# Kernel tuning notes

Hardware: AMD Instinct MI355X
Metric: run time of the kernel (lower is better)

The kernel has to match this reference:

```python
import math
import jax, jax.numpy as jnp
import numpy as np

NUM_EXPERTS = 8
TOP_K = 2
HIDDEN = 1024
INTERMEDIATE = 4096
CAPACITY_FACTOR = 1.0


def setup_inputs() -> dict:
    key = jax.random.key(0)
    k1, k2, k3, k4, k5, k6 = jax.random.split(key, 6)
    T = 8192
    hidden_states = jax.random.normal(k1, (T, HIDDEN), dtype=jnp.float32)
    # router affinities (already softmax-normalized in the real pipeline; uniform here is fine for correctness)
    expert_affinities = jax.random.uniform(k2, (T, NUM_EXPERTS), dtype=jnp.float32)
    expert_index = jax.random.randint(k3, (T, TOP_K), 0, NUM_EXPERTS, dtype=jnp.int32)
    scale = 0.02
    gate_w = jax.random.normal(k4, (NUM_EXPERTS, HIDDEN, INTERMEDIATE), dtype=jnp.float32) * scale
    up_w = jax.random.normal(k5, (NUM_EXPERTS, HIDDEN, INTERMEDIATE), dtype=jnp.float32) * scale
    down_w = jax.random.normal(k6, (NUM_EXPERTS, INTERMEDIATE, HIDDEN), dtype=jnp.float32) * scale
    return {"hidden_states": hidden_states, "expert_affinities": expert_affinities,
            "gate_w": gate_w, "up_w": up_w, "down_w": down_w, "expert_index": expert_index}


def reference(hidden_states, expert_affinities, gate_w, up_w, down_w, expert_index):
    T, H = hidden_states.shape
    E, K = NUM_EXPERTS, TOP_K
    C = min(math.ceil(T * K * CAPACITY_FACTOR / E), T)  # expert capacity (static)

    # top_k-hot expert mask (T, E)
    expert_mask = jax.nn.one_hot(expert_index, E, dtype=jnp.float32).sum(axis=1)
    # 1-indexed position of each token within each expert's queue
    position_in_expert = jnp.cumsum(expert_mask, axis=0)
    # capacity-based token dropping
    expert_mask = jnp.where(position_in_expert > C, 0.0, expert_mask)

    # masked (and L1-normalized) affinities of chosen experts
    aff_masked = jnp.where(expert_mask == 0, 0.0, expert_affinities)
    denom = jnp.maximum(jnp.sum(jnp.abs(aff_masked), axis=1, keepdims=True), 1e-12)
    aff_masked = aff_masked / denom  # normalize_top_k_affinities=True

    # flattened slot index per (token, expert): expert e occupies slots [e*C, (e+1)*C)
    offsets = jnp.arange(E, dtype=jnp.float32) * C
    pos_off = position_in_expert + offsets[None, :]
    pos_off = jnp.where(expert_mask == 0, 0.0, pos_off)

    # (T, K) slot index (1-based; 0 == dropped)
    perm_idx = jnp.take_along_axis(pos_off, expert_index, axis=1).astype(jnp.int32)

    # invert permutation: slot -> token (1-based; slot 0 collects all dropped tokens, then discarded)
    tok_ids = jnp.broadcast_to((jnp.arange(T, dtype=jnp.int32) + 1)[:, None], (T, K)).reshape(-1)
    assign = jnp.zeros(E * C + 1, dtype=jnp.int32).at[perm_idx.reshape(-1)].set(tok_ids)
    assign = assign[1:].reshape(E, C) - 1
    assign = jnp.maximum(assign, 0)          # empty slots read token 0 (output unused)
    perm_idx = jnp.maximum(perm_idx - 1, 0)  # dropped tokens read slot 0 (affinity == 0)

    # gather tokens into per-expert blocks and run grouped GLU MLP
    x_e = hidden_states[assign]  # (E, C, H)
    gate = jax.nn.silu(jnp.einsum('ech,ehi->eci', x_e, gate_w))
    inter = gate * jnp.einsum('ech,ehi->eci', x_e, up_w)  # (E, C, I)
    out_e = jnp.einsum('eci,eih->ech', inter, down_w)      # (E, C, H)
    permuted_output = out_e.reshape(E * C, H)

    # combine: gather each token's top_k expert outputs weighted by masked affinities
    out_k = permuted_output[perm_idx]                                   # (T, K, H)
    aff_k = jnp.take_along_axis(aff_masked, expert_index, axis=1)       # (T, K)
    return jnp.sum(out_k * aff_k[:, :, None], axis=1)
```

## Files before the change

kernel.cpp:

```cpp
#include <hip/hip_runtime.h>
#include <stdint.h>

#define T_TOK 8192
#define HID   1024
#define INTER 4096
#define NE    8
#define TOPK  2
#define CAP   2048
#define EC    (NE * CAP)


typedef __attribute__((ext_vector_type(8))) short bf16x8;
typedef __attribute__((ext_vector_type(4))) float f32x4;

static __device__ __forceinline__ unsigned short f2bf(float f) {
    union { float f; unsigned u; } a; a.f = f;
    unsigned r = a.u + 0x7FFFu + ((a.u >> 16) & 1u);
    return (unsigned short)(r >> 16);
}
static __device__ __forceinline__ float bf2f(unsigned short b) {
    union { unsigned u; float f; } a; a.u = ((unsigned)b) << 16;
    return a.f;
}

static __device__ __forceinline__ void gload(const unsigned short* g, unsigned short* l) {
    __builtin_amdgcn_global_load_lds((__attribute__((address_space(1))) void*)(uintptr_t)g,
                                     (__attribute__((address_space(3))) void*)l, 16, 0, 0);
}

#define BAR() do { asm volatile("" ::: "memory"); __builtin_amdgcn_s_barrier(); asm volatile("" ::: "memory"); } while (0)
#define WAITVM(N) asm volatile("s_waitcnt vmcnt(" #N ")" ::: "memory")

__global__ __launch_bounds__(512) void route_kernel(const int* __restrict__ eidx,
                                                    int* __restrict__ perm,
                                                    int* __restrict__ assign) {
    int tid = threadIdx.x;
    for (int i = tid; i < EC; i += 512) assign[i] = 0;
    __syncthreads();
    int e = tid >> 6;
    int lane = tid & 63;
    const int TPL = T_TOK / 64;
    int t0 = lane * TPL;
    int cnt = 0;
    for (int t = t0; t < t0 + TPL; ++t) {
        int e0 = eidx[t * 2], e1 = eidx[t * 2 + 1];
        cnt += (e0 == e) + (e1 == e);
    }
    int incl = cnt;
    #pragma unroll
    for (int off = 1; off < 64; off <<= 1) {
        int n = __shfl_up(incl, off, 64);
        if (lane >= off) incl += n;
    }
    int run = incl - cnt;
    for (int t = t0; t < t0 + TPL; ++t) {
        int e0 = eidx[t * 2], e1 = eidx[t * 2 + 1];
        int c = (e0 == e) + (e1 == e);
        if (c) {
            run += c;
            int pos = run;
            bool keep = (pos <= CAP);
            int pi = keep ? (pos + e * CAP) : 0;
            if (e0 == e) perm[t * 2]     = pi;
            if (e1 == e) perm[t * 2 + 1] = pi;
            if (keep) assign[pi - 1] = t;
        }
    }
}

__global__ __launch_bounds__(256) void transpose_cvt2(const float* __restrict__ in0,
                                                      unsigned short* __restrict__ out0,
                                                      const float* __restrict__ in1,
                                                      unsigned short* __restrict__ out1) {
    __shared__ unsigned short tile[64][68];
    int z = blockIdx.z;
    const float* in = (z < 8) ? in0 : in1;
    unsigned short* out = (z < 8) ? out0 : out1;
    int e = z & 7;
    const int R = HID, Cc = INTER;
    const float* inp = in + (size_t)e * R * Cc;
    unsigned short* outp = out + (size_t)e * R * Cc;
    int c0 = blockIdx.x * 64, r0 = blockIdx.y * 64;
    int t = threadIdx.x;
    int x = t & 15;
    int ry = t >> 4;
    #pragma unroll
    for (int j = 0; j < 4; ++j) {
        int row = ry + 16 * j;
        float4 v = *(const float4*)(inp + (size_t)(r0 + row) * Cc + c0 + 4 * x);
        ushort4 o;
        o.x = f2bf(v.x); o.y = f2bf(v.y); o.z = f2bf(v.z); o.w = f2bf(v.w);
        *(ushort4*)&tile[row][4 * x] = o;
    }
    __syncthreads();
    #pragma unroll
    for (int j = 0; j < 4; ++j) {
        int oc = ry + 16 * j;
        ushort4 o;
        o.x = tile[4 * x + 0][oc];
        o.y = tile[4 * x + 1][oc];
        o.z = tile[4 * x + 2][oc];
        o.w = tile[4 * x + 3][oc];
        *(ushort4*)(outp + (size_t)(c0 + oc) * R + r0 + 4 * x) = o;
    }
}

__global__ __launch_bounds__(256) void transpose_cvt(const float* __restrict__ in,
                                                     unsigned short* __restrict__ out,
                                                     int R, int Cc) {
    __shared__ unsigned short tile[64][68];
    int e = blockIdx.z;
    const float* inp = in + (size_t)e * R * Cc;
    unsigned short* outp = out + (size_t)e * R * Cc;
    int c0 = blockIdx.x * 64, r0 = blockIdx.y * 64;
    int t = threadIdx.x;
    int x = t & 15;
    int ry = t >> 4;
    #pragma unroll
    for (int j = 0; j < 4; ++j) {
        int row = ry + 16 * j;
        float4 v = *(const float4*)(inp + (size_t)(r0 + row) * Cc + c0 + 4 * x);
        ushort4 o;
        o.x = f2bf(v.x); o.y = f2bf(v.y); o.z = f2bf(v.z); o.w = f2bf(v.w);
        *(ushort4*)&tile[row][4 * x] = o;
    }
    __syncthreads();
    #pragma unroll
    for (int j = 0; j < 4; ++j) {
        int oc = ry + 16 * j;
        ushort4 o;
        o.x = tile[4 * x + 0][oc];
        o.y = tile[4 * x + 1][oc];
        o.z = tile[4 * x + 2][oc];
        o.w = tile[4 * x + 3][oc];
        *(ushort4*)(outp + (size_t)(c0 + oc) * R + r0 + 4 * x) = o;
    }
}

__global__ __launch_bounds__(256) void gather_cvt(const float* __restrict__ hs,
                                                  const int* __restrict__ assign,
                                                  unsigned short* __restrict__ xe) {
    int s = blockIdx.x;
    int tok = assign[s];
    const float* src = hs + (size_t)tok * HID;
    unsigned short* dst = xe + (size_t)s * HID;
    int h = threadIdx.x * 4;
    float4 v = *(const float4*)(src + h);
    ushort4 o;
    o.x = f2bf(v.x); o.y = f2bf(v.y); o.z = f2bf(v.z); o.w = f2bf(v.w);
    *(ushort4*)(dst + h) = o;
}


#define BUFE 12288

#define MFMA16(ACC, O, B0, B1) \
    _Pragma("unroll") \
    for (int mi = 0; mi < 8; ++mi) { \
        ACC[mi][O]     = __builtin_amdgcn_mfma_f32_16x16x32_bf16(aF[mi], B0, ACC[mi][O], 0, 0, 0); \
        ACC[mi][O + 1] = __builtin_amdgcn_mfma_f32_16x16x32_bf16(aF[mi], B1, ACC[mi][O + 1], 0, 0, 0); \
    }

#define LOAD_AF(rd) \
    _Pragma("unroll") \
    for (int mi = 0; mi < 8; ++mi) aF[mi] = *(const bf16x8*)((rd) + aRd + mi * 512);

__global__ __launch_bounds__(256, 2) void gateup_gemm(const unsigned short* __restrict__ Xe,
                                                      const unsigned short* __restrict__ WgT,
                                                      const unsigned short* __restrict__ WuT,
                                                      unsigned short* __restrict__ interB) {
    extern __shared__ __align__(16) unsigned short smemU[];
    const int K = HID;
    const int NT = K / 32;

    int e  = blockIdx.x;
    int m0 = blockIdx.y * 256;
    int n0 = blockIdx.z * 64;

    int tid = threadIdx.x;
    int lane = tid & 63, w = tid >> 6;
    int lm = lane & 15, hi = lane >> 4;
    int wm = w >> 1, wn = w & 1;

    const int swz  = (hi ^ ((lm >> 1) & 3)) << 3;
    const int aRd  = (wm * 128 + lm) * 32 + swz;
    const int r1Rd = 8192  + (wn * 32 + lm) * 32 + swz;
    const int r2Rd = 10240 + (wn * 32 + lm) * 32 + swz;

    int sr = lane >> 2;
    int sc = ((lane & 3) ^ ((lane >> 3) & 3)) << 3;
    const unsigned short* aS = Xe  + ((size_t)e * CAP   + m0 + w * 64 + sr) * K + sc;
    const unsigned short* gS = WgT + ((size_t)e * INTER + n0 + w * 16 + sr) * K + sc;
    const unsigned short* uS = WuT + ((size_t)e * INTER + n0 + w * 16 + sr) * K + sc;
    const int dA = w * 2048;
    const int dG = 8192  + w * 512;
    const int dU = 10240 + w * 512;

    f32x4 zero = {0.f, 0.f, 0.f, 0.f};
    f32x4 accG[8][2], accU[8][2];
    #pragma unroll
    for (int i = 0; i < 8; ++i) {
        accG[i][0] = zero; accG[i][1] = zero;
        accU[i][0] = zero; accU[i][1] = zero;
    }

    unsigned short* p0 = smemU;
    unsigned short* p1 = smemU + BUFE;
    unsigned short* p2 = smemU + 2 * BUFE;

    {
        #pragma unroll
        for (int j = 0; j < 4; ++j) gload(aS + (size_t)j * 16 * K, p0 + dA + j * 512);
        gload(gS, p0 + dG); gload(uS, p0 + dU);
        #pragma unroll
        for (int j = 0; j < 4; ++j) gload(aS + (size_t)j * 16 * K + 32, p1 + dA + j * 512);
        gload(gS + 32, p1 + dG); gload(uS + 32, p1 + dU);
        WAITVM(7);
        BAR();
    }

    bf16x8 aF[8];
    int gk = 64;
    for (int t = 0; t < NT - 2; ++t) {
        const unsigned short* rd = p0;
        unsigned short* wr = p2;
        LOAD_AF(rd);
        bf16x8 b0 = *(const bf16x8*)(rd + r1Rd);
        bf16x8 b1 = *(const bf16x8*)(rd + r1Rd + 512);
        #pragma unroll
        for (int j = 0; j < 4; ++j) gload(aS + (size_t)j * 16 * K + gk, wr + dA + j * 512);
        gload(gS + gk, wr + dG);
        WAITVM(11);
        BAR();
        __builtin_amdgcn_s_setprio(1);
        MFMA16(accG, 0, b0, b1);
        __builtin_amdgcn_s_setprio(0);
        BAR();
        b0 = *(const bf16x8*)(rd + r2Rd);
        b1 = *(const bf16x8*)(rd + r2Rd + 512);
        gload(uS + gk, wr + dU);
        WAITVM(7);
        BAR();
        __builtin_amdgcn_s_setprio(1);
        MFMA16(accU, 0, b0, b1);
        __builtin_amdgcn_s_setprio(0);
        BAR();
        unsigned short* tmp = p0; p0 = p1; p1 = p2; p2 = tmp;
        gk += 32;
    }
    {
        const unsigned short* rd = p0;
        LOAD_AF(rd);
        bf16x8 b0 = *(const bf16x8*)(rd + r1Rd);
        bf16x8 b1 = *(const bf16x8*)(rd + r1Rd + 512);
        WAITVM(6);
        BAR();
        MFMA16(accG, 0, b0, b1);
        BAR();
        b0 = *(const bf16x8*)(rd + r2Rd);
        b1 = *(const bf16x8*)(rd + r2Rd + 512);
        WAITVM(1);
        BAR();
        MFMA16(accU, 0, b0, b1);
        BAR();
    }
    {
        const unsigned short* rd = p1;
        LOAD_AF(rd);
        bf16x8 b0 = *(const bf16x8*)(rd + r1Rd);
        bf16x8 b1 = *(const bf16x8*)(rd + r1Rd + 512);
        WAITVM(0);
        BAR();
        MFMA16(accG, 0, b0, b1);
        BAR();
        b0 = *(const bf16x8*)(rd + r2Rd);
        b1 = *(const bf16x8*)(rd + r2Rd + 512);
        MFMA16(accU, 0, b0, b1);
    }

    __syncthreads();
    unsigned short* bounce = smemU;
    #pragma unroll
    for (int mi = 0; mi < 8; ++mi)
        #pragma unroll
        for (int nf = 0; nf < 2; ++nf) {
            f32x4 g4 = accG[mi][nf], u4 = accU[mi][nf];
            #pragma unroll
            for (int r = 0; r < 4; ++r) {
                int row = wm * 128 + mi * 16 + hi * 4 + r;
                int col = wn * 32 + nf * 16 + lm;
                float g = g4[r];
                float s = g / (1.f + __expf(-g)) * u4[r];
                bounce[row * 72 + col] = f2bf(s);
            }
        }
    __syncthreads();
    {
        unsigned short* Op = interB + ((size_t)e * CAP + m0) * INTER + n0;
        int rr = tid >> 3, cc = (tid & 7) * 8;
        #pragma unroll
        for (int j = 0; j < 8; ++j) {
            int row = rr + 32 * j;
            bf16x8 v = *(const bf16x8*)&bounce[row * 72 + cc];
            *(bf16x8*)(Op + (size_t)row * INTER + cc) = v;
        }
    }
}

__global__ __launch_bounds__(256, 2) void down_gemm(const unsigned short* __restrict__ interB,
                                                    const unsigned short* __restrict__ WdT,
                                                    unsigned short* __restrict__ pout) {
    extern __shared__ __align__(16) unsigned short smemU[];
    const int K = INTER;
    const int NT = K / 32;

    int e  = blockIdx.x;
    int m0 = blockIdx.y * 256;
    int n0 = blockIdx.z * 128;

    int tid = threadIdx.x;
    int lane = tid & 63, w = tid >> 6;
    int lm = lane & 15, hi = lane >> 4;
    int wm = w >> 1, wn = w & 1;

    const int swz  = (hi ^ ((lm >> 1) & 3)) << 3;
    const int aRd  = (wm * 128 + lm) * 32 + swz;
    const int r1Rd = 8192  + (wn * 32 + lm) * 32 + swz;
    const int r2Rd = 10240 + (wn * 32 + lm) * 32 + swz;

    int sr = lane >> 2;
    int sc = ((lane & 3) ^ ((lane >> 3) & 3)) << 3;
    const unsigned short* aS = interB + ((size_t)e * CAP + m0 + w * 64 + sr) * K + sc;
    int rb1 = (w >> 1) * 64 + (w & 1) * 16;
    const unsigned short* b1S = WdT + ((size_t)e * HID + n0 + rb1 + sr) * K + sc;
    const unsigned short* b2S = WdT + ((size_t)e * HID + n0 + rb1 + 32 + sr) * K + sc;
    const int dA = w * 2048;
    const int d1 = 8192  + w * 512;
    const int d2 = 10240 + w * 512;

    f32x4 zero = {0.f, 0.f, 0.f, 0.f};
    f32x4 acc[8][4];
    #pragma unroll
    for (int i = 0; i < 8; ++i)
        #pragma unroll
        for (int j = 0; j < 4; ++j) acc[i][j] = zero;

    unsigned short* p0 = smemU;
    unsigned short* p1 = smemU + BUFE;
    unsigned short* p2 = smemU + 2 * BUFE;

    {
        #pragma unroll
        for (int j = 0; j < 4; ++j) gload(aS + (size_t)j * 16 * K, p0 + dA + j * 512);
        gload(b1S, p0 + d1); gload(b2S, p0 + d2);
        #pragma unroll
        for (int j = 0; j < 4; ++j) gload(aS + (size_t)j * 16 * K + 32, p1 + dA + j * 512);
        gload(b1S + 32, p1 + d1); gload(b2S + 32, p1 + d2);
        WAITVM(7);
        BAR();
    }

    bf16x8 aF[8];
    int gk = 64;
    for (int t = 0; t < NT - 2; ++t) {
        const unsigned short* rd = p0;
        unsigned short* wr = p2;
        LOAD_AF(rd);
        bf16x8 b0 = *(const bf16x8*)(rd + r1Rd);
        bf16x8 b1 = *(const bf16x8*)(rd + r1Rd + 512);
        #pragma unroll
        for (int j = 0; j < 4; ++j) gload(aS + (size_t)j * 16 * K + gk, wr + dA + j * 512);
        gload(b1S + gk, wr + d1);
        WAITVM(11);
        BAR();
        __builtin_amdgcn_s_setprio(1);
        MFMA16(acc, 0, b0, b1);
        __builtin_amdgcn_s_setprio(0);
        BAR();
        b0 = *(const bf16x8*)(rd + r2Rd);
        b1 = *(const bf16x8*)(rd + r2Rd + 512);
        gload(b2S + gk, wr + d2);
        WAITVM(7);
        BAR();
        __builtin_amdgcn_s_setprio(1);
        MFMA16(acc, 2, b0, b1);
        __builtin_amdgcn_s_setprio(0);
        BAR();
        unsigned short* tmp = p0; p0 = p1; p1 = p2; p2 = tmp;
        gk += 32;
    }
    {
        const unsigned short* rd = p0;
        LOAD_AF(rd);
        bf16x8 b0 = *(const bf16x8*)(rd + r1Rd);
        bf16x8 b1 = *(const bf16x8*)(rd + r1Rd + 512);
        WAITVM(6);
        BAR();
        MFMA16(acc, 0, b0, b1);
        BAR();
        b0 = *(const bf16x8*)(rd + r2Rd);
        b1 = *(const bf16x8*)(rd + r2Rd + 512);
        WAITVM(1);
        BAR();
        MFMA16(acc, 2, b0, b1);
        BAR();
    }
    {
        const unsigned short* rd = p1;
        LOAD_AF(rd);
        bf16x8 b0 = *(const bf16x8*)(rd + r1Rd);
        bf16x8 b1 = *(const bf16x8*)(rd + r1Rd + 512);
        WAITVM(0);
        BAR();
        MFMA16(acc, 0, b0, b1);
        BAR();
        b0 = *(const bf16x8*)(rd + r2Rd);
        b1 = *(const bf16x8*)(rd + r2Rd + 512);
        MFMA16(acc, 2, b0, b1);
    }

    unsigned short* bounce = smemU;
    unsigned short* Op = pout + ((size_t)e * CAP + m0) * HID + n0;
    int rr = tid >> 3, c8 = tid & 7;
    int colp = c8 * 8;
    #pragma unroll
    for (int R = 0; R < 2; ++R) {
        __syncthreads();
        #pragma unroll
        for (int mi = 0; mi < 8; ++mi)
            #pragma unroll
            for (int nf = 0; nf < 2; ++nf) {
                f32x4 a4 = acc[mi][2 * R + nf];
                #pragma unroll
                for (int r = 0; r < 4; ++r) {
                    int row = wm * 128 + mi * 16 + hi * 4 + r;
                    int col = wn * 32 + nf * 16 + lm;
                    bounce[row * 72 + col] = f2bf(a4[r]);
                }
            }
        __syncthreads();
        int gcol = (colp >> 5) * 64 + R * 32 + (colp & 31);
        #pragma unroll
        for (int j = 0; j < 8; ++j) {
            int row = rr + 32 * j;
            bf16x8 v = *(const bf16x8*)&bounce[row * 72 + colp];
            *(bf16x8*)(Op + (size_t)row * HID + gcol) = v;
        }
    }
}

__global__ __launch_bounds__(256) void combine_kernel(const float* __restrict__ aff,
                                                      const int* __restrict__ eidx,
                                                      const int* __restrict__ perm,
                                                      const unsigned short* __restrict__ pout,
                                                      float* __restrict__ out) {
    int t = blockIdx.x;
    int e0 = eidx[t * 2], e1 = eidx[t * 2 + 1];
    int p0 = perm[t * 2], p1 = perm[t * 2 + 1];
    bool k0 = p0 > 0, k1 = p1 > 0;
    float a0 = aff[t * NE + e0], a1 = aff[t * NE + e1];
    float denom = (k0 ? fabsf(a0) : 0.f) + ((e1 != e0 && k1) ? fabsf(a1) : 0.f);
    denom = fmaxf(denom, 1e-12f);
    float w0 = k0 ? a0 / denom : 0.f;
    float w1 = k1 ? a1 / denom : 0.f;
    int s0 = k0 ? p0 - 1 : 0;
    int s1 = k1 ? p1 - 1 : 0;
    int h = threadIdx.x * 4;
    ushort4 v0 = *(const ushort4*)(pout + (size_t)s0 * HID + h);
    ushort4 v1 = *(const ushort4*)(pout + (size_t)s1 * HID + h);
    float4 o;
    o.x = w0 * bf2f(v0.x) + w1 * bf2f(v1.x);
    o.y = w0 * bf2f(v0.y) + w1 * bf2f(v1.y);
    o.z = w0 * bf2f(v0.z) + w1 * bf2f(v1.z);
    o.w = w0 * bf2f(v0.w) + w1 * bf2f(v1.w);
    *(float4*)(out + (size_t)t * HID + h) = o;
}

extern "C" void kernel_launch(void* const* d_in, const int* in_sizes, int n_in,
                              void* d_out, int out_size, void* d_ws, size_t ws_size,
                              hipStream_t stream) {
    (void)in_sizes; (void)n_in; (void)out_size; (void)ws_size;
    const float* hs   = (const float*)d_in[0];
    const float* aff  = (const float*)d_in[1];
    const float* gw   = (const float*)d_in[2];
    const float* uw   = (const float*)d_in[3];
    const float* dw   = (const float*)d_in[4];
    const int*   eidx = (const int*)d_in[5];
    float* out = (float*)d_out;

    char* ws = (char*)d_ws;
    unsigned short* WgT    = (unsigned short*)(ws);
    unsigned short* WuT    = (unsigned short*)(ws + ((size_t)64  << 20));
    unsigned short* WdT    = (unsigned short*)(ws + ((size_t)128 << 20));
    unsigned short* Xe     = (unsigned short*)(ws + ((size_t)192 << 20));
    unsigned short* interB = (unsigned short*)(ws + ((size_t)224 << 20));
    unsigned short* pout   = (unsigned short*)(ws + ((size_t)352 << 20));
    int*            perm   = (int*)           (ws + ((size_t)416 << 20));
    int*            assign = perm + (T_TOK * TOPK);

    static int attr_set = 0;
    if (!attr_set) {
        (void)hipFuncSetAttribute((const void*)gateup_gemm,
                                  hipFuncAttributeMaxDynamicSharedMemorySize, 73728);
        (void)hipFuncSetAttribute((const void*)down_gemm,
                                  hipFuncAttributeMaxDynamicSharedMemorySize, 73728);
        attr_set = 1;
    }

    route_kernel<<<1, 512, 0, stream>>>(eidx, perm, assign);
    transpose_cvt2<<<dim3(INTER / 64, HID / 64, 16), 256, 0, stream>>>(uw, WuT, gw, WgT);
    transpose_cvt<<<dim3(HID / 64, INTER / 64, NE), 256, 0, stream>>>(dw, WdT, INTER, HID);
    gather_cvt<<<EC, 256, 0, stream>>>(hs, assign, Xe);
    gateup_gemm<<<dim3(8, 8, 64), 256, 73728, stream>>>(Xe, WgT, WuT, interB);
    down_gemm<<<dim3(8, 8, 8), 256, 73728, stream>>>(interB, WdT, pout);
    combine_kernel<<<T_TOK, 256, 0, stream>>>(aff, eidx, perm, pout, out);
}
```

Before: 912.0 us.

## Switch expert GEMMs to 32x32x16 MFMA and load B operands directly from global

Both the gate/up and down GEMMs move from 16x16x32 bf16 MFMA tiles to 32x32x16 tiles with 16-wide accumulators. Weight (B) fragments are now read straight from global memory into registers and prefetched one K-step ahead, instead of being staged through LDS. Only the activation tile stays in LDS, which shrinks shared memory per block from 72KB to 48KB and removes one barrier pair per K-step. In exchange, the B reads become uncoalesced per-lane global loads that depend on cache hits, and the epilogue row mapping changes to match the new accumulator layout.

```diff
diff --git a/kernel.cpp b/kernel.cpp
--- a/kernel.cpp
+++ b/kernel.cpp
@@ -12,6 +12,7 @@
 
 typedef __attribute__((ext_vector_type(8))) short bf16x8;
 typedef __attribute__((ext_vector_type(4))) float f32x4;
+typedef __attribute__((ext_vector_type(16))) float f32x16;
 
 static __device__ __forceinline__ unsigned short f2bf(float f) {
     union { float f; unsigned u; } a; a.f = f;
@@ -152,18 +153,7 @@
 }
 
 
-#define BUFE 12288
-
-#define MFMA16(ACC, O, B0, B1) \
-    _Pragma("unroll") \
-    for (int mi = 0; mi < 8; ++mi) { \
-        ACC[mi][O]     = __builtin_amdgcn_mfma_f32_16x16x32_bf16(aF[mi], B0, ACC[mi][O], 0, 0, 0); \
-        ACC[mi][O + 1] = __builtin_amdgcn_mfma_f32_16x16x32_bf16(aF[mi], B1, ACC[mi][O + 1], 0, 0, 0); \
-    }
-
-#define LOAD_AF(rd) \
-    _Pragma("unroll") \
-    for (int mi = 0; mi < 8; ++mi) aF[mi] = *(const bf16x8*)((rd) + aRd + mi * 512);
+#define BUFE 8192
 
 __global__ __launch_bounds__(256, 2) void gateup_gemm(const unsigned short* __restrict__ Xe,
                                                       const unsigned short* __restrict__ WgT,
@@ -179,121 +169,123 @@
 
     int tid = threadIdx.x;
     int lane = tid & 63, w = tid >> 6;
-    int lm = lane & 15, hi = lane >> 4;
+    int r = lane & 31, hi2 = lane >> 5;
     int wm = w >> 1, wn = w & 1;
 
-    const int swz  = (hi ^ ((lm >> 1) & 3)) << 3;
-    const int aRd  = (wm * 128 + lm) * 32 + swz;
-    const int r1Rd = 8192  + (wn * 32 + lm) * 32 + swz;
-    const int r2Rd = 10240 + (wn * 32 + lm) * 32 + swz;
+    int q = (r >> 1) & 3;
+    const int aOff0 = wm * 4096 + r * 32 + ((hi2 ^ q) << 3);
+    const int aOff1 = wm * 4096 + r * 32 + (((2 | hi2) ^ q) << 3);
 
     int sr = lane >> 2;
     int sc = ((lane & 3) ^ ((lane >> 3) & 3)) << 3;
-    const unsigned short* aS = Xe  + ((size_t)e * CAP   + m0 + w * 64 + sr) * K + sc;
-    const unsigned short* gS = WgT + ((size_t)e * INTER + n0 + w * 16 + sr) * K + sc;
-    const unsigned short* uS = WuT + ((size_t)e * INTER + n0 + w * 16 + sr) * K + sc;
+    const unsigned short* aS = Xe + ((size_t)e * CAP + m0 + w * 64 + sr) * K + sc;
     const int dA = w * 2048;
-    const int dG = 8192  + w * 512;
-    const int dU = 10240 + w * 512;
-
-    f32x4 zero = {0.f, 0.f, 0.f, 0.f};
-    f32x4 accG[8][2], accU[8][2];
-    #pragma unroll
-    for (int i = 0; i < 8; ++i) {
-        accG[i][0] = zero; accG[i][1] = zero;
-        accU[i][0] = zero; accU[i][1] = zero;
-    }
+
+    const unsigned short* gP = WgT + ((size_t)e * INTER + n0 + wn * 32 + r) * K + hi2 * 8;
+    const unsigned short* uP = WuT + ((size_t)e * INTER + n0 + wn * 32 + r) * K + hi2 * 8;
+
+    f32x16 accG[4], accU[4];
+    f32x16 zero = {0.f,0.f,0.f,0.f,0.f,0.f,0.f,0.f,0.f,0.f,0.f,0.f,0.f,0.f,0.f,0.f};
+    #pragma unroll
+    for (int i = 0; i < 4; ++i) { accG[i] = zero; accU[i] = zero; }
 
     unsigned short* p0 = smemU;
     unsigned short* p1 = smemU + BUFE;
     unsigned short* p2 = smemU + 2 * BUFE;
 
-    {
-        #pragma unroll
-        for (int j = 0; j < 4; ++j) gload(aS + (size_t)j * 16 * K, p0 + dA + j * 512);
-        gload(gS, p0 + dG); gload(uS, p0 + dU);
-        #pragma unroll
-        for (int j = 0; j < 4; ++j) gload(aS + (size_t)j * 16 * K + 32, p1 + dA + j * 512);
-        gload(gS + 32, p1 + dG); gload(uS + 32, p1 + dU);
-        WAITVM(7);
-        BAR();
-    }
-
-    bf16x8 aF[8];
+    #pragma unroll
+    for (int j = 0; j < 4; ++j) gload(aS + (size_t)j * 16 * K, p0 + dA + j * 512);
+    #pragma unroll
+    for (int j = 0; j < 4; ++j) gload(aS + (size_t)j * 16 * K + 32, p1 + dA + j * 512);
+    bf16x8 bG0 = *(const bf16x8*)(gP);
+    bf16x8 bG1 = *(const bf16x8*)(gP + 16);
+    bf16x8 bU0 = *(const bf16x8*)(uP);
+    bf16x8 bU1 = *(const bf16x8*)(uP + 16);
+    WAITVM(8);
+    BAR();
+
+    bf16x8 aF0[4], aF1[4];
     int gk = 64;
     for (int t = 0; t < NT - 2; ++t) {
-        const unsigned short* rd = p0;
-        unsigned short* wr = p2;
-        LOAD_AF(rd);
-        bf16x8 b0 = *(const bf16x8*)(rd + r1Rd);
-        bf16x8 b1 = *(const bf16x8*)(rd + r1Rd + 512);
-        #pragma unroll
-        for (int j = 0; j < 4; ++j) gload(aS + (size_t)j * 16 * K + gk, wr + dA + j * 512);
-        gload(gS + gk, wr + dG);
-        WAITVM(11);
+        #pragma unroll
+        for (int mi = 0; mi < 4; ++mi) aF0[mi] = *(const bf16x8*)(p0 + aOff0 + mi * 1024);
+        #pragma unroll
+        for (int j = 0; j < 4; ++j) gload(aS + (size_t)j * 16 * K + gk, p2 + dA + j * 512);
+        WAITVM(4);
         BAR();
         __builtin_amdgcn_s_setprio(1);
-        MFMA16(accG, 0, b0, b1);
+        #pragma unroll
+        for (int mi = 0; mi < 4; ++mi) aF1[mi] = *(const bf16x8*)(p0 + aOff1 + mi * 1024);
+        bf16x8 nG0 = *(const bf16x8*)(gP + 32);
+        bf16x8 nG1 = *(const bf16x8*)(gP + 48);
+        bf16x8 nU0 = *(const bf16x8*)(uP + 32);
+        bf16x8 nU1 = *(const bf16x8*)(uP + 48);
+        #pragma unroll
+        for (int mi = 0; mi < 4; ++mi) {
+            accG[mi] = __builtin_amdgcn_mfma_f32_32x32x16_bf16(aF0[mi], bG0, accG[mi], 0, 0, 0);
+            accU[mi] = __builtin_amdgcn_mfma_f32_32x32x16_bf16(aF0[mi], bU0, accU[mi], 0, 0, 0);
+        }
+        #pragma unroll
+        for (int mi = 0; mi < 4; ++mi) {
+            accG[mi] = __builtin_amdgcn_mfma_f32_32x32x16_bf16(aF1[mi], bG1, accG[mi], 0, 0, 0);
+            accU[mi] = __builtin_amdgcn_mfma_f32_32x32x16_bf16(aF1[mi], bU1, accU[mi], 0, 0, 0);
+        }
         __builtin_amdgcn_s_setprio(0);
         BAR();
-        b0 = *(const bf16x8*)(rd + r2Rd);
-        b1 = *(const bf16x8*)(rd + r2Rd + 512);
-        gload(uS + gk, wr + dU);
-        WAITVM(7);
-        BAR();
-        __builtin_amdgcn_s_setprio(1);
-        MFMA16(accU, 0, b0, b1);
-        __builtin_amdgcn_s_setprio(0);
-        BAR();
+        bG0 = nG0; bG1 = nG1; bU0 = nU0; bU1 = nU1;
+        gP += 32; uP += 32;
         unsigned short* tmp = p0; p0 = p1; p1 = p2; p2 = tmp;
         gk += 32;
     }
     {
-        const unsigned short* rd = p0;
-        LOAD_AF(rd);
-        bf16x8 b0 = *(const bf16x8*)(rd + r1Rd);
-        bf16x8 b1 = *(const bf16x8*)(rd + r1Rd + 512);
-        WAITVM(6);
-        BAR();
-        MFMA16(accG, 0, b0, b1);
-        BAR();
-        b0 = *(const bf16x8*)(rd + r2Rd);
-        b1 = *(const bf16x8*)(rd + r2Rd + 512);
-        WAITVM(1);
-        BAR();
-        MFMA16(accU, 0, b0, b1);
-        BAR();
+        #pragma unroll
+        for (int mi = 0; mi < 4; ++mi) aF0[mi] = *(const bf16x8*)(p0 + aOff0 + mi * 1024);
+        WAITVM(0);
+        BAR();
+        #pragma unroll
+        for (int mi = 0; mi < 4; ++mi) aF1[mi] = *(const bf16x8*)(p0 + aOff1 + mi * 1024);
+        bf16x8 nG0 = *(const bf16x8*)(gP + 32);
+        bf16x8 nG1 = *(const bf16x8*)(gP + 48);
+        bf16x8 nU0 = *(const bf16x8*)(uP + 32);
+        bf16x8 nU1 = *(const bf16x8*)(uP + 48);
+        #pragma unroll
+        for (int mi = 0; mi < 4; ++mi) {
+            accG[mi] = __builtin_amdgcn_mfma_f32_32x32x16_bf16(aF0[mi], bG0, accG[mi], 0, 0, 0);
+            accU[mi] = __builtin_amdgcn_mfma_f32_32x32x16_bf16(aF0[mi], bU0, accU[mi], 0, 0, 0);
+            accG[mi] = __builtin_amdgcn_mfma_f32_32x32x16_bf16(aF1[mi], bG1, accG[mi], 0, 0, 0);
+            accU[mi] = __builtin_amdgcn_mfma_f32_32x32x16_bf16(aF1[mi], bU1, accU[mi], 0, 0, 0);
+        }
+        BAR();
+        bG0 = nG0; bG1 = nG1; bU0 = nU0; bU1 = nU1;
     }
     {
-        const unsigned short* rd = p1;
-        LOAD_AF(rd);
-        bf16x8 b0 = *(const bf16x8*)(rd + r1Rd);
-        bf16x8 b1 = *(const bf16x8*)(rd + r1Rd + 512);
-        WAITVM(0);
-        BAR();
-        MFMA16(accG, 0, b0, b1);
-        BAR();
-        b0 = *(const bf16x8*)(rd + r2Rd);
-        b1 = *(const bf16x8*)(rd + r2Rd + 512);
-        MFMA16(accU, 0, b0, b1);
+        #pragma unroll
+        for (int mi = 0; mi < 4; ++mi) aF0[mi] = *(const bf16x8*)(p1 + aOff0 + mi * 1024);
+        #pragma unroll
+        for (int mi = 0; mi < 4; ++mi) aF1[mi] = *(const bf16x8*)(p1 + aOff1 + mi * 1024);
+        #pragma unroll
+        for (int mi = 0; mi < 4; ++mi) {
+            accG[mi] = __builtin_amdgcn_mfma_f32_32x32x16_bf16(aF0[mi], bG0, accG[mi], 0, 0, 0);
+            accU[mi] = __builtin_amdgcn_mfma_f32_32x32x16_bf16(aF0[mi], bU0, accU[mi], 0, 0, 0);
+            accG[mi] = __builtin_amdgcn_mfma_f32_32x32x16_bf16(aF1[mi], bG1, accG[mi], 0, 0, 0);
+            accU[mi] = __builtin_amdgcn_mfma_f32_32x32x16_bf16(aF1[mi], bU1, accU[mi], 0, 0, 0);
+        }
     }
 
     __syncthreads();
     unsigned short* bounce = smemU;
-    #pragma unroll
-    for (int mi = 0; mi < 8; ++mi)
-        #pragma unroll
-        for (int nf = 0; nf < 2; ++nf) {
-            f32x4 g4 = accG[mi][nf], u4 = accU[mi][nf];
-            #pragma unroll
-            for (int r = 0; r < 4; ++r) {
-                int row = wm * 128 + mi * 16 + hi * 4 + r;
-                int col = wn * 32 + nf * 16 + lm;
-                float g = g4[r];
-                float s = g / (1.f + __expf(-g)) * u4[r];
-                bounce[row * 72 + col] = f2bf(s);
-            }
-        }
+    int col = wn * 32 + r;
+    #pragma unroll
+    for (int mi = 0; mi < 4; ++mi) {
+        f32x16 g16 = accG[mi], u16 = accU[mi];
+        #pragma unroll
+        for (int rg = 0; rg < 16; ++rg) {
+            int row = wm * 128 + mi * 32 + (rg & 3) + 8 * (rg >> 2) + 4 * hi2;
+            float g = g16[rg];
+            float s = g / (1.f + __expf(-g)) * u16[rg];
+            bounce[row * 72 + col] = f2bf(s);
+        }
+    }
     __syncthreads();
     {
         unsigned short* Op = interB + ((size_t)e * CAP + m0) * INTER + n0;
@@ -320,124 +312,125 @@
 
     int tid = threadIdx.x;
     int lane = tid & 63, w = tid >> 6;
-    int lm = lane & 15, hi = lane >> 4;
+    int r = lane & 31, hi2 = lane >> 5;
     int wm = w >> 1, wn = w & 1;
 
-    const int swz  = (hi ^ ((lm >> 1) & 3)) << 3;
-    const int aRd  = (wm * 128 + lm) * 32 + swz;
-    const int r1Rd = 8192  + (wn * 32 + lm) * 32 + swz;
-    const int r2Rd = 10240 + (wn * 32 + lm) * 32 + swz;
+    int q = (r >> 1) & 3;
+    const int aOff0 = wm * 4096 + r * 32 + ((hi2 ^ q) << 3);
+    const int aOff1 = wm * 4096 + r * 32 + (((2 | hi2) ^ q) << 3);
 
     int sr = lane >> 2;
     int sc = ((lane & 3) ^ ((lane >> 3) & 3)) << 3;
     const unsigned short* aS = interB + ((size_t)e * CAP + m0 + w * 64 + sr) * K + sc;
-    int rb1 = (w >> 1) * 64 + (w & 1) * 16;
-    const unsigned short* b1S = WdT + ((size_t)e * HID + n0 + rb1 + sr) * K + sc;
-    const unsigned short* b2S = WdT + ((size_t)e * HID + n0 + rb1 + 32 + sr) * K + sc;
     const int dA = w * 2048;
-    const int d1 = 8192  + w * 512;
-    const int d2 = 10240 + w * 512;
-
-    f32x4 zero = {0.f, 0.f, 0.f, 0.f};
-    f32x4 acc[8][4];
-    #pragma unroll
-    for (int i = 0; i < 8; ++i)
-        #pragma unroll
-        for (int j = 0; j < 4; ++j) acc[i][j] = zero;
+
+    const unsigned short* dP0 = WdT + ((size_t)e * HID + n0 + wn * 64 + r) * K + hi2 * 8;
+    const unsigned short* dP1 = dP0 + (size_t)32 * K;
+
+    f32x16 acc[4][2];
+    f32x16 zero = {0.f,0.f,0.f,0.f,0.f,0.f,0.f,0.f,0.f,0.f,0.f,0.f,0.f,0.f,0.f,0.f};
+    #pragma unroll
+    for (int i = 0; i < 4; ++i) { acc[i][0] = zero; acc[i][1] = zero; }
 
     unsigned short* p0 = smemU;
     unsigned short* p1 = smemU + BUFE;
     unsigned short* p2 = smemU + 2 * BUFE;
 
-    {
-        #pragma unroll
-        for (int j = 0; j < 4; ++j) gload(aS + (size_t)j * 16 * K, p0 + dA + j * 512);
-        gload(b1S, p0 + d1); gload(b2S, p0 + d2);
-        #pragma unroll
-        for (int j = 0; j < 4; ++j) gload(aS + (size_t)j * 16 * K + 32, p1 + dA + j * 512);
-        gload(b1S + 32, p1 + d1); gload(b2S + 32, p1 + d2);
-        WAITVM(7);
-        BAR();
-    }
-
-    bf16x8 aF[8];
+    #pragma unroll
+    for (int j = 0; j < 4; ++j) gload(aS + (size_t)j * 16 * K, p0 + dA + j * 512);
+    #pragma unroll
+    for (int j = 0; j < 4; ++j) gload(aS + (size_t)j * 16 * K + 32, p1 + dA + j * 512);
+    bf16x8 b00 = *(const bf16x8*)(dP0);
+    bf16x8 b01 = *(const bf16x8*)(dP0 + 16);
+    bf16x8 b10 = *(const bf16x8*)(dP1);
+    bf16x8 b11 = *(const bf16x8*)(dP1 + 16);
+    WAITVM(8);
+    BAR();
+
+    bf16x8 aF0[4], aF1[4];
     int gk = 64;
     for (int t = 0; t < NT - 2; ++t) {
-        const unsigned short* rd = p0;
-        unsigned short* wr = p2;
-        LOAD_AF(rd);
-        bf16x8 b0 = *(const bf16x8*)(rd + r1Rd);
-        bf16x8 b1 = *(const bf16x8*)(rd + r1Rd + 512);
-        #pragma unroll
-        for (int j = 0; j < 4; ++j) gload(aS + (size_t)j * 16 * K + gk, wr + dA + j * 512);
-        gload(b1S + gk, wr + d1);
-        WAITVM(11);
+        #pragma unroll
+        for (int mi = 0; mi < 4; ++mi) aF0[mi] = *(const bf16x8*)(p0 + aOff0 + mi * 1024);
+        #pragma unroll
+        for (int j = 0; j < 4; ++j) gload(aS + (size_t)j * 16 * K + gk, p2 + dA + j * 512);
+        WAITVM(4);
         BAR();
         __builtin_amdgcn_s_setprio(1);
-        MFMA16(acc, 0, b0, b1);
+        #pragma unroll
+        for (int mi = 0; mi < 4; ++mi) aF1[mi] = *(const bf16x8*)(p0 + aOff1 + mi * 1024);
+        bf16x8 n00 = *(const bf16x8*)(dP0 + 32);
+        bf16x8 n01 = *(const bf16x8*)(dP0 + 48);
+        bf16x8 n10 = *(const bf16x8*)(dP1 + 32);
+        bf16x8 n11 = *(const bf16x8*)(dP1 + 48);
+        #pragma unroll
+        for (int mi = 0; mi < 4; ++mi) {
+            acc[mi][0] = __builtin_amdgcn_mfma_f32_32x32x16_bf16(aF0[mi], b00, acc[mi][0], 0, 0, 0);
+            acc[mi][1] = __builtin_amdgcn_mfma_f32_32x32x16_bf16(aF0[mi], b10, acc[mi][1], 0, 0, 0);
+        }
+        #pragma unroll
+        for (int mi = 0; mi < 4; ++mi) {
+            acc[mi][0] = __builtin_amdgcn_mfma_f32_32x32x16_bf16(aF1[mi], b01, acc[mi][0], 0, 0, 0);
+            acc[mi][1] = __builtin_amdgcn_mfma_f32_32x32x16_bf16(aF1[mi], b11, acc[mi][1], 0, 0, 0);
+        }
         __builtin_amdgcn_s_setprio(0);
         BAR();
-        b0 = *(const bf16x8*)(rd + r2Rd);
-        b1 = *(const bf16x8*)(rd + r2Rd + 512);
-        gload(b2S + gk, wr + d2);
-        WAITVM(7);
-        BAR();
-        __builtin_amdgcn_s_setprio(1);
-        MFMA16(acc, 2, b0, b1);
-        __builtin_amdgcn_s_setprio(0);
-        BAR();
+        b00 = n00; b01 = n01; b10 = n10; b11 = n11;
+        dP0 += 32; dP1 += 32;
         unsigned short* tmp = p0; p0 = p1; p1 = p2; p2 = tmp;
         gk += 32;
     }
     {
-        const unsigned short* rd = p0;
-        LOAD_AF(rd);
-        bf16x8 b0 = *(const bf16x8*)(rd + r1Rd);
-        bf16x8 b1 = *(const bf16x8*)(rd + r1Rd + 512);
-        WAITVM(6);
-        BAR();
-        MFMA16(acc, 0, b0, b1);
-        BAR();
-        b0 = *(const bf16x8*)(rd + r2Rd);
-        b1 = *(const bf16x8*)(rd + r2Rd + 512);
-        WAITVM(1);
-        BAR();
-        MFMA16(acc, 2, b0, b1);
-        BAR();
+        #pragma unroll
+        for (int mi = 0; mi < 4; ++mi) aF0[mi] = *(const bf16x8*)(p0 + aOff0 + mi * 1024);
+        WAITVM(0);
+        BAR();
+        #pragma unroll
+        for (int mi = 0; mi < 4; ++mi) aF1[mi] = *(const bf16x8*)(p0 + aOff1 + mi * 1024);
+        bf16x8 n00 = *(const bf16x8*)(dP0 + 32);
+        bf16x8 n01 = *(const bf16x8*)(dP0 + 48);
+        bf16x8 n10 = *(const bf16x8*)(dP1 + 32);
+        bf16x8 n11 = *(const bf16x8*)(dP1 + 48);
+        #pragma unroll
+        for (int mi = 0; mi < 4; ++mi) {
+            acc[mi][0] = __builtin_amdgcn_mfma_f32_32x32x16_bf16(aF0[mi], b00, acc[mi][0], 0, 0, 0);
+            acc[mi][1] = __builtin_amdgcn_mfma_f32_32x32x16_bf16(aF0[mi], b10, acc[mi][1], 0, 0, 0);
+            acc[mi][0] = __builtin_amdgcn_mfma_f32_32x32x16_bf16(aF1[mi], b01, acc[mi][0], 0, 0, 0);
+            acc[mi][1] = __builtin_amdgcn_mfma_f32_32x32x16_bf16(aF1[mi], b11, acc[mi][1], 0, 0, 0);
+        }
+        BAR();
+        b00 = n00; b01 = n01; b10 = n10; b11 = n11;
     }
     {
-        const unsigned short* rd = p1;
-        LOAD_AF(rd);
-        bf16x8 b0 = *(const bf16x8*)(rd + r1Rd);
-        bf16x8 b1 = *(const bf16x8*)(rd + r1Rd + 512);
-        WAITVM(0);
-        BAR();
-        MFMA16(acc, 0, b0, b1);
-        BAR();
-        b0 = *(const bf16x8*)(rd + r2Rd);
-        b1 = *(const bf16x8*)(rd + r2Rd + 512);
-        MFMA16(acc, 2, b0, b1);
+        #pragma unroll
+        for (int mi = 0; mi < 4; ++mi) aF0[mi] = *(const bf16x8*)(p1 + aOff0 + mi * 1024);
+        #pragma unroll
+        for (int mi = 0; mi < 4; ++mi) aF1[mi] = *(const bf16x8*)(p1 + aOff1 + mi * 1024);
+        #pragma unroll
+        for (int mi = 0; mi < 4; ++mi) {
+            acc[mi][0] = __builtin_amdgcn_mfma_f32_32x32x16_bf16(aF0[mi], b00, acc[mi][0], 0, 0, 0);
+            acc[mi][1] = __builtin_amdgcn_mfma_f32_32x32x16_bf16(aF0[mi], b10, acc[mi][1], 0, 0, 0);
+            acc[mi][0] = __builtin_amdgcn_mfma_f32_32x32x16_bf16(aF1[mi], b01, acc[mi][0], 0, 0, 0);
+            acc[mi][1] = __builtin_amdgcn_mfma_f32_32x32x16_bf16(aF1[mi], b11, acc[mi][1], 0, 0, 0);
+        }
     }
 
     unsigned short* bounce = smemU;
     unsigned short* Op = pout + ((size_t)e * CAP + m0) * HID + n0;
-    int rr = tid >> 3, c8 = tid & 7;
-    int colp = c8 * 8;
+    int rr = tid >> 3, colp = (tid & 7) * 8;
+    int colc = wn * 32 + r;
     #pragma unroll
     for (int R = 0; R < 2; ++R) {
         __syncthreads();
         #pragma unroll
-        for (int mi = 0; mi < 8; ++mi)
+        for (int mi = 0; mi < 4; ++mi) {
+            f32x16 a16 = acc[mi][R];
             #pragma unroll
-            for (int nf = 0; nf < 2; ++nf) {
-                f32x4 a4 = acc[mi][2 * R + nf];
-                #pragma unroll
-                for (int r = 0; r < 4; ++r) {
-                    int row = wm * 128 + mi * 16 + hi * 4 + r;
-                    int col = wn * 32 + nf * 16 + lm;
-                    bounce[row * 72 + col] = f2bf(a4[r]);
-                }
+            for (int rg = 0; rg < 16; ++rg) {
+                int row = wm * 128 + mi * 32 + (rg & 3) + 8 * (rg >> 2) + 4 * hi2;
+                bounce[row * 72 + colc] = f2bf(a16[rg]);
             }
+        }
         __syncthreads();
         int gcol = (colp >> 5) * 64 + R * 32 + (colp & 31);
         #pragma unroll
@@ -501,9 +494,9 @@
     static int attr_set = 0;
     if (!attr_set) {
         (void)hipFuncSetAttribute((const void*)gateup_gemm,
-                                  hipFuncAttributeMaxDynamicSharedMemorySize, 73728);
+                                  hipFuncAttributeMaxDynamicSharedMemorySize, 49152);
         (void)hipFuncSetAttribute((const void*)down_gemm,
-                                  hipFuncAttributeMaxDynamicSharedMemorySize, 73728);
+                                  hipFuncAttributeMaxDynamicSharedMemorySize, 49152);
         attr_set = 1;
     }
 
@@ -511,7 +504,7 @@
     transpose_cvt2<<<dim3(INTER / 64, HID / 64, 16), 256, 0, stream>>>(uw, WuT, gw, WgT);
     transpose_cvt<<<dim3(HID / 64, INTER / 64, NE), 256, 0, stream>>>(dw, WdT, INTER, HID);
     gather_cvt<<<EC, 256, 0, stream>>>(hs, assign, Xe);
-    gateup_gemm<<<dim3(8, 8, 64), 256, 73728, stream>>>(Xe, WgT, WuT, interB);
-    down_gemm<<<dim3(8, 8, 8), 256, 73728, stream>>>(interB, WdT, pout);
+    gateup_gemm<<<dim3(8, 8, 64), 256, 49152, stream>>>(Xe, WgT, WuT, interB);
+    down_gemm<<<dim3(8, 8, 8), 256, 49152, stream>>>(interB, WdT, pout);
     combine_kernel<<<T_TOK, 256, 0, stream>>>(aff, eidx, perm, pout, out);
 }
```

Result: slower. 1.143 ms (+25.4%).
